# Optimization experiments

Hardware: AMD Instinct MI355X
Metric: run time of the kernel (lower is better)

The kernel has to match this reference:

```python
import jax, jax.numpy as jnp
import numpy as np

B, F, D, DENSE, CARD = 16384, 26, 64, 13, 100000
H_BOT, H_TOP = 8, 16  # hardcoded hidden sizes in the torch module


def setup_inputs() -> dict:
    key = jax.random.key(0)
    ks = jax.random.split(key, 12)
    dense_x = jax.random.normal(ks[0], (B, DENSE), dtype=jnp.float32)
    sparse_x = jax.random.randint(ks[1], (B, F), 0, CARD, dtype=jnp.int64)
    # all tables share cardinality -> stack into one [F, CARD, D] tensor
    tables = jax.random.normal(ks[2], (F, CARD, D), dtype=jnp.float32) * 0.01
    # bottom MLP: dense_dim -> 8 -> embedding_dim
    w1 = jax.random.normal(ks[3], (DENSE, H_BOT), dtype=jnp.float32) * (1.0 / np.sqrt(DENSE))
    b1 = jnp.zeros((H_BOT,), dtype=jnp.float32)
    w2 = jax.random.normal(ks[4], (H_BOT, D), dtype=jnp.float32) * (1.0 / np.sqrt(H_BOT))
    b2 = jnp.zeros((D,), dtype=jnp.float32)
    # top MLP: F*D + D -> 16 -> 1, sigmoid
    top_in = F * D + D
    tw1 = jax.random.normal(ks[5], (top_in, H_TOP), dtype=jnp.float32) * (1.0 / np.sqrt(top_in))
    tb1 = jnp.zeros((H_TOP,), dtype=jnp.float32)
    tw2 = jax.random.normal(ks[6], (H_TOP, 1), dtype=jnp.float32) * (1.0 / np.sqrt(H_TOP))
    tb2 = jnp.zeros((1,), dtype=jnp.float32)
    return {"dense_x": dense_x, "sparse_x": sparse_x, "tables": tables,
            "w1": w1, "b1": b1, "w2": w2, "b2": b2,
            "tw1": tw1, "tb1": tb1, "tw2": tw2, "tb2": tb2}


def reference(dense_x, sparse_x, tables, w1, b1, w2, b2, tw1, tb1, tw2, tb2):
    # bottom MLP
    dense_out = jnp.maximum(dense_x @ w1 + b1, 0.0) @ w2 + b2  # [B, D]
    # per-table gather, vectorized over the F tables
    emb = jax.vmap(lambda t, idx: t[idx], in_axes=(0, 1), out_axes=1)(tables, sparse_x)  # [B, F, D]
    interaction = jnp.concatenate([emb.reshape(emb.shape[0], -1), dense_out], axis=1)  # [B, F*D + D]
    # top MLP
    logits = jnp.maximum(interaction @ tw1 + tb1, 0.0) @ tw2 + tb2  # [B, 1]
    return jax.nn.sigmoid(logits)
```

## Files before the change

kernel.cpp:

```cpp
#include <hip/hip_runtime.h>
#include <hip/hip_bf16.h>
#include <cmath>

typedef __bf16 bf16_t;
typedef bf16_t bf16x8 __attribute__((ext_vector_type(8)));
typedef float floatx4 __attribute__((ext_vector_type(4)));

#define NFEAT 26
#define DIM 64
#define DENSE_IN 13
#define CARD 100000
#define HBOT 8
#define KSTEPS 54

__global__ __launch_bounds__(256, 1) void dlrm_fused(
    const float* __restrict__ dense_x,
    const int* __restrict__ sparse_x,
    const float* __restrict__ tables,
    const float* __restrict__ w1, const float* __restrict__ b1,
    const float* __restrict__ w2, const float* __restrict__ b2,
    const float* __restrict__ tw1, const float* __restrict__ tb1,
    const float* __restrict__ tw2, const float* __restrict__ tb2,
    float* __restrict__ out)
{
    __shared__ __align__(16) bf16_t Blds[KSTEPS * 64 * 8];
    __shared__ __align__(16) bf16_t Dlds[4 * 2 * 64 * 8];
    __shared__ int idx_lds[64 * NFEAT];

    const int tid   = threadIdx.x;
    const int block = blockIdx.x;
    const int lane  = tid & 63;
    const int wave  = tid >> 6;

    const int* sp = sparse_x + (long)block * 64 * NFEAT;
    for (int i = tid; i < 64 * NFEAT; i += 256) idx_lds[i] = sp[i];

    for (int slot = tid; slot < KSTEPS * 64; slot += 256) {
        int t  = slot >> 6;
        int l  = slot & 63;
        int n  = l & 15;
        int k0 = t * 32 + (l >> 4) * 8;
        bf16x8 v;
        #pragma unroll
        for (int j = 0; j < 8; ++j)
            v[j] = (bf16_t)tw1[(k0 + j) * 16 + n];
        *(bf16x8*)(&Blds[slot * 8]) = v;
    }

    for (int slot = tid; slot < 512; slot += 256) {
        int tile = slot >> 7;
        int tp   = (slot >> 6) & 1;
        int l    = slot & 63;
        int m    = l & 15;
        int q    = l >> 4;
        int s    = block * 64 + tile * 16 + m;
        int d0   = tp * 32 + q * 8;
        float x[DENSE_IN];
        #pragma unroll
        for (int i = 0; i < DENSE_IN; ++i) x[i] = dense_x[s * DENSE_IN + i];
        float h8[HBOT];
        #pragma unroll
        for (int j = 0; j < HBOT; ++j) {
            float acc = b1[j];
            #pragma unroll
            for (int i = 0; i < DENSE_IN; ++i) acc = fmaf(x[i], w1[i * HBOT + j], acc);
            h8[j] = fmaxf(acc, 0.f);
        }
        bf16x8 v;
        #pragma unroll
        for (int jj = 0; jj < 8; ++jj) {
            float acc = b2[d0 + jj];
            #pragma unroll
            for (int j = 0; j < HBOT; ++j) acc = fmaf(h8[j], w2[j * DIM + d0 + jj], acc);
            v[jj] = (bf16_t)acc;
        }
        *(bf16x8*)(&Dlds[slot * 8]) = v;
    }

    __syncthreads();

    const int tile = wave;
    const int m    = lane & 15;
    const int q    = lane >> 4;
    floatx4 acc = {0.f, 0.f, 0.f, 0.f};

    const int* myidx = &idx_lds[(tile * 16 + m) * NFEAT];

    #pragma unroll 2
    for (int f = 0; f < NFEAT; ++f) {
        int idx = myidx[f];
        const float* row = tables + (long)(f * CARD + idx) * DIM;
        #pragma unroll
        for (int h = 0; h < 2; ++h) {
            const float4 p0 = *(const float4*)(row + h * 32 + q * 8);
            const float4 p1 = *(const float4*)(row + h * 32 + q * 8 + 4);
            bf16x8 a;
            a[0] = (bf16_t)p0.x; a[1] = (bf16_t)p0.y;
            a[2] = (bf16_t)p0.z; a[3] = (bf16_t)p0.w;
            a[4] = (bf16_t)p1.x; a[5] = (bf16_t)p1.y;
            a[6] = (bf16_t)p1.z; a[7] = (bf16_t)p1.w;
            bf16x8 b = *(bf16x8*)(&Blds[((f * 2 + h) * 64 + lane) * 8]);
            acc = __builtin_amdgcn_mfma_f32_16x16x32_bf16(a, b, acc, 0, 0, 0);
        }
    }
    #pragma unroll
    for (int tp = 0; tp < 2; ++tp) {
        bf16x8 a = *(bf16x8*)(&Dlds[((tile * 2 + tp) * 64 + lane) * 8]);
        bf16x8 b = *(bf16x8*)(&Blds[((52 + tp) * 64 + lane) * 8]);
        acc = __builtin_amdgcn_mfma_f32_16x16x32_bf16(a, b, acc, 0, 0, 0);
    }

    const int h = lane & 15;
    const float bias = tb1[h];
    const float wout = tw2[h];
    float p[4];
    #pragma unroll
    for (int i = 0; i < 4; ++i) p[i] = fmaxf(acc[i] + bias, 0.f) * wout;
    #pragma unroll
    for (int off = 1; off < 16; off <<= 1) {
        #pragma unroll
        for (int i = 0; i < 4; ++i) p[i] += __shfl_xor(p[i], off, 64);
    }
    if (h == 0) {
        const float bout = tb2[0];
        #pragma unroll
        for (int i = 0; i < 4; ++i) {
            float logit = p[i] + bout;
            out[block * 64 + tile * 16 + q * 4 + i] = 1.f / (1.f + expf(-logit));
        }
    }
}

extern "C" void kernel_launch(void* const* d_in, const int* in_sizes, int n_in,
                              void* d_out, int out_size, void* d_ws, size_t ws_size,
                              hipStream_t stream) {
    const float* dense_x = (const float*)d_in[0];
    const int*   sparse_x = (const int*)d_in[1];
    const float* tables  = (const float*)d_in[2];
    const float* w1  = (const float*)d_in[3];
    const float* b1  = (const float*)d_in[4];
    const float* w2  = (const float*)d_in[5];
    const float* b2  = (const float*)d_in[6];
    const float* tw1 = (const float*)d_in[7];
    const float* tb1 = (const float*)d_in[8];
    const float* tw2 = (const float*)d_in[9];
    const float* tb2 = (const float*)d_in[10];
    float* out = (float*)d_out;

    dlrm_fused<<<256, 256, 0, stream>>>(dense_x, sparse_x, tables,
                                        w1, b1, w2, b2,
                                        tw1, tb1, tw2, tb2, out);
}
```

Measured before the change: 751.4 us.

## Split K across waves with 16-row blocks and precompute tw1 fragments

Moves the bf16 conversion of tw1 into a separate prep kernel that writes to workspace, so each block no longer rebuilds the full B fragment in LDS. The main kernel now handles 16 samples per block across 1024 blocks. The four waves split the 54 K-steps between them and reduce their partial accumulators through LDS. This raises the number of gather loads in flight and occupancy (launch bounds allow 4 blocks per CU), at the cost of an extra launch, a cross-wave reduction, and B fragments read from global/L2 rather than LDS.

```diff
diff --git a/kernel.cpp b/kernel.cpp
--- a/kernel.cpp
+++ b/kernel.cpp
@@ -1,5 +1,4 @@
 #include <hip/hip_runtime.h>
-#include <hip/hip_bf16.h>
 #include <cmath>
 
 typedef __bf16 bf16_t;
@@ -13,120 +12,118 @@
 #define HBOT 8
 #define KSTEPS 54
 
-__global__ __launch_bounds__(256, 1) void dlrm_fused(
+__global__ __launch_bounds__(256) void prep_bfrag(
+    const float* __restrict__ tw1, bf16_t* __restrict__ bws)
+{
+    int slot = blockIdx.x * 256 + threadIdx.x;
+    if (slot >= KSTEPS * 64) return;
+    int t  = slot >> 6;
+    int l  = slot & 63;
+    int n  = l & 15;
+    int k0 = t * 32 + (l >> 4) * 8;
+    bf16x8 v;
+    #pragma unroll
+    for (int j = 0; j < 8; ++j) v[j] = (bf16_t)tw1[(k0 + j) * 16 + n];
+    *(bf16x8*)(&bws[slot * 8]) = v;
+}
+
+__global__ __launch_bounds__(256, 4) void dlrm_main(
     const float* __restrict__ dense_x,
-    const int* __restrict__ sparse_x,
+    const int*   __restrict__ sparse_x,
     const float* __restrict__ tables,
     const float* __restrict__ w1, const float* __restrict__ b1,
     const float* __restrict__ w2, const float* __restrict__ b2,
-    const float* __restrict__ tw1, const float* __restrict__ tb1,
-    const float* __restrict__ tw2, const float* __restrict__ tb2,
+    const bf16_t* __restrict__ bws,
+    const float* __restrict__ tb1, const float* __restrict__ tw2,
+    const float* __restrict__ tb2,
     float* __restrict__ out)
 {
-    __shared__ __align__(16) bf16_t Blds[KSTEPS * 64 * 8];
-    __shared__ __align__(16) bf16_t Dlds[4 * 2 * 64 * 8];
-    __shared__ int idx_lds[64 * NFEAT];
+    __shared__ int idx_lds[16 * NFEAT];
+    __shared__ floatx4 red[3][64];
 
-    const int tid   = threadIdx.x;
-    const int block = blockIdx.x;
-    const int lane  = tid & 63;
-    const int wave  = tid >> 6;
+    const int tid  = threadIdx.x;
+    const int blk  = blockIdx.x;
+    const int lane = tid & 63;
+    const int w    = tid >> 6;
+    const int m    = lane & 15;
+    const int q    = lane >> 4;
 
-    const int* sp = sparse_x + (long)block * 64 * NFEAT;
-    for (int i = tid; i < 64 * NFEAT; i += 256) idx_lds[i] = sp[i];
+    const int* sp = sparse_x + blk * 16 * NFEAT;
+    for (int i = tid; i < 16 * NFEAT; i += 256) idx_lds[i] = sp[i];
 
-    for (int slot = tid; slot < KSTEPS * 64; slot += 256) {
-        int t  = slot >> 6;
-        int l  = slot & 63;
-        int n  = l & 15;
-        int k0 = t * 32 + (l >> 4) * 8;
-        bf16x8 v;
-        #pragma unroll
-        for (int j = 0; j < 8; ++j)
-            v[j] = (bf16_t)tw1[(k0 + j) * 16 + n];
-        *(bf16x8*)(&Blds[slot * 8]) = v;
-    }
+    floatx4 acc = {0.f, 0.f, 0.f, 0.f};
 
-    for (int slot = tid; slot < 512; slot += 256) {
-        int tile = slot >> 7;
-        int tp   = (slot >> 6) & 1;
-        int l    = slot & 63;
-        int m    = l & 15;
-        int q    = l >> 4;
-        int s    = block * 64 + tile * 16 + m;
-        int d0   = tp * 32 + q * 8;
+    if (w < 2) {
+        const float* dx = dense_x + (blk * 16 + m) * DENSE_IN;
         float x[DENSE_IN];
         #pragma unroll
-        for (int i = 0; i < DENSE_IN; ++i) x[i] = dense_x[s * DENSE_IN + i];
+        for (int i = 0; i < DENSE_IN; ++i) x[i] = dx[i];
         float h8[HBOT];
         #pragma unroll
         for (int j = 0; j < HBOT; ++j) {
-            float acc = b1[j];
+            float a0 = b1[j];
             #pragma unroll
-            for (int i = 0; i < DENSE_IN; ++i) acc = fmaf(x[i], w1[i * HBOT + j], acc);
-            h8[j] = fmaxf(acc, 0.f);
+            for (int i = 0; i < DENSE_IN; ++i) a0 = fmaf(x[i], w1[i * HBOT + j], a0);
+            h8[j] = fmaxf(a0, 0.f);
         }
-        bf16x8 v;
+        const int d0 = w * 32 + q * 8;
+        bf16x8 a;
         #pragma unroll
         for (int jj = 0; jj < 8; ++jj) {
-            float acc = b2[d0 + jj];
+            float a0 = b2[d0 + jj];
             #pragma unroll
-            for (int j = 0; j < HBOT; ++j) acc = fmaf(h8[j], w2[j * DIM + d0 + jj], acc);
-            v[jj] = (bf16_t)acc;
+            for (int j = 0; j < HBOT; ++j) a0 = fmaf(h8[j], w2[j * DIM + d0 + jj], a0);
+            a[jj] = (bf16_t)a0;
         }
-        *(bf16x8*)(&Dlds[slot * 8]) = v;
+        bf16x8 b = *(const bf16x8*)(bws + ((52 + w) * 64 + lane) * 8);
+        acc = __builtin_amdgcn_mfma_f32_16x16x32_bf16(a, b, acc, 0, 0, 0);
     }
 
     __syncthreads();
 
-    const int tile = wave;
-    const int m    = lane & 15;
-    const int q    = lane >> 4;
-    floatx4 acc = {0.f, 0.f, 0.f, 0.f};
-
-    const int* myidx = &idx_lds[(tile * 16 + m) * NFEAT];
-
-    #pragma unroll 2
-    for (int f = 0; f < NFEAT; ++f) {
-        int idx = myidx[f];
-        const float* row = tables + (long)(f * CARD + idx) * DIM;
-        #pragma unroll
-        for (int h = 0; h < 2; ++h) {
-            const float4 p0 = *(const float4*)(row + h * 32 + q * 8);
-            const float4 p1 = *(const float4*)(row + h * 32 + q * 8 + 4);
-            bf16x8 a;
-            a[0] = (bf16_t)p0.x; a[1] = (bf16_t)p0.y;
-            a[2] = (bf16_t)p0.z; a[3] = (bf16_t)p0.w;
-            a[4] = (bf16_t)p1.x; a[5] = (bf16_t)p1.y;
-            a[6] = (bf16_t)p1.z; a[7] = (bf16_t)p1.w;
-            bf16x8 b = *(bf16x8*)(&Blds[((f * 2 + h) * 64 + lane) * 8]);
-            acc = __builtin_amdgcn_mfma_f32_16x16x32_bf16(a, b, acc, 0, 0, 0);
-        }
-    }
+    const int* myidx = &idx_lds[m * NFEAT];
     #pragma unroll
-    for (int tp = 0; tp < 2; ++tp) {
-        bf16x8 a = *(bf16x8*)(&Dlds[((tile * 2 + tp) * 64 + lane) * 8]);
-        bf16x8 b = *(bf16x8*)(&Blds[((52 + tp) * 64 + lane) * 8]);
+    for (int u = 0; u < 13; ++u) {
+        const int t = w + 4 * u;
+        const int f = t >> 1;
+        const int h = t & 1;
+        const int idx = myidx[f];
+        const float* row = tables + (f * CARD + idx) * DIM + h * 32 + q * 8;
+        const float4 p0 = *(const float4*)(row);
+        const float4 p1 = *(const float4*)(row + 4);
+        bf16x8 a;
+        a[0] = (bf16_t)p0.x; a[1] = (bf16_t)p0.y;
+        a[2] = (bf16_t)p0.z; a[3] = (bf16_t)p0.w;
+        a[4] = (bf16_t)p1.x; a[5] = (bf16_t)p1.y;
+        a[6] = (bf16_t)p1.z; a[7] = (bf16_t)p1.w;
+        bf16x8 b = *(const bf16x8*)(bws + (t * 64 + lane) * 8);
         acc = __builtin_amdgcn_mfma_f32_16x16x32_bf16(a, b, acc, 0, 0, 0);
     }
 
-    const int h = lane & 15;
-    const float bias = tb1[h];
-    const float wout = tw2[h];
-    float p[4];
-    #pragma unroll
-    for (int i = 0; i < 4; ++i) p[i] = fmaxf(acc[i] + bias, 0.f) * wout;
-    #pragma unroll
-    for (int off = 1; off < 16; off <<= 1) {
+    if (w > 0) red[w - 1][lane] = acc;
+    __syncthreads();
+    if (w == 0) {
+        acc += red[0][lane];
+        acc += red[1][lane];
+        acc += red[2][lane];
+        const float bias = tb1[m];
+        const float wout = tw2[m];
+        float p[4];
         #pragma unroll
-        for (int i = 0; i < 4; ++i) p[i] += __shfl_xor(p[i], off, 64);
-    }
-    if (h == 0) {
-        const float bout = tb2[0];
+        for (int i = 0; i < 4; ++i) p[i] = fmaxf(acc[i] + bias, 0.f) * wout;
         #pragma unroll
-        for (int i = 0; i < 4; ++i) {
-            float logit = p[i] + bout;
-            out[block * 64 + tile * 16 + q * 4 + i] = 1.f / (1.f + expf(-logit));
+        for (int off = 1; off < 16; off <<= 1) {
+            #pragma unroll
+            for (int i = 0; i < 4; ++i) p[i] += __shfl_xor(p[i], off, 64);
+        }
+        if (m == 0) {
+            const float bout = tb2[0];
+            float4 o;
+            o.x = 1.f / (1.f + expf(-(p[0] + bout)));
+            o.y = 1.f / (1.f + expf(-(p[1] + bout)));
+            o.z = 1.f / (1.f + expf(-(p[2] + bout)));
+            o.w = 1.f / (1.f + expf(-(p[3] + bout)));
+            *(float4*)(out + blk * 16 + q * 4) = o;
         }
     }
 }
@@ -146,8 +143,10 @@
     const float* tw2 = (const float*)d_in[9];
     const float* tb2 = (const float*)d_in[10];
     float* out = (float*)d_out;
+    bf16_t* bws = (bf16_t*)d_ws;
 
-    dlrm_fused<<<256, 256, 0, stream>>>(dense_x, sparse_x, tables,
-                                        w1, b1, w2, b2,
-                                        tw1, tb1, tw2, tb2, out);
+    prep_bfrag<<<(KSTEPS * 64 + 255) / 256, 256, 0, stream>>>(tw1, bws);
+    dlrm_main<<<16384 / 16, 256, 0, stream>>>(dense_x, sparse_x, tables,
+                                              w1, b1, w2, b2, bws,
+                                              tb1, tw2, tb2, out);
 }
```

Result: no change. 742.2 us (-1.2%).
